# Optimization experiments

Hardware: AMD Instinct MI355X
Metric: run time of the kernel (lower is better)

Reference implementation:

```python
import jax, jax.numpy as jnp
from jax import lax
import numpy as np

TOPN = 6
IOU_THRESH = 0.25
PAD = 224
CROP = 224

def make_edge_anchors():
    # (fm, stride, base_size, scales, ratios): 6 anchors/cell on 14x14 and 7x7, 9 on 4x4
    specs = [(14, 32, 48, [1.0, 1.26], [0.667, 1.0, 1.5]),
             (7, 64, 96, [1.0, 1.26], [0.667, 1.0, 1.5]),
             (4, 112, 192, [1.0, 1.26, 1.59], [0.667, 1.0, 1.5])]
    out = []
    for fm, stride, base, scales, ratios in specs:
        cy = (np.arange(fm) + 0.5) * stride
        yy, xx = np.meshgrid(cy, cy, indexing='ij')
        for s in scales:          # anchor-type-major order matches NCHW flatten of tidy heads
            for r in ratios:
                h = base * s * np.sqrt(r)
                w = base * s / np.sqrt(r)
                b = np.stack([yy - h / 2, xx - w / 2, yy + h / 2, xx + w / 2], -1)
                out.append(b.reshape(-1, 4))
    anchors = np.concatenate(out, 0) + PAD  # shift into padded-image coords
    return np.clip(anchors, 0, 448 + 2 * PAD).astype(np.int32)  # [1614,4]

def conv2d(x, w, b, stride, pad):
    y = lax.conv_general_dilated(x, w, (stride, stride), [(pad, pad), (pad, pad)],
                                 dimension_numbers=('NCHW', 'OIHW', 'NCHW'))
    return y + b[None, :, None, None]

def proposal_net(rpn_feature, w1, b1, w2, b2, w3, b3, tw1, tb1, tw2, tb2, tw3, tb3):
    B = rpn_feature.shape[0]
    d1 = jax.nn.relu(conv2d(rpn_feature, w1, b1, 1, 1))  # [B,128,14,14]
    d2 = jax.nn.relu(conv2d(d1, w2, b2, 2, 1))           # [B,128,7,7]
    d3 = jax.nn.relu(conv2d(d2, w3, b3, 2, 1))           # [B,128,4,4]
    t1 = conv2d(d1, tw1, tb1, 1, 0).reshape(B, -1)       # [B,1176]
    t2 = conv2d(d2, tw2, tb2, 1, 0).reshape(B, -1)       # [B,294]
    t3 = conv2d(d3, tw3, tb3, 1, 0).reshape(B, -1)       # [B,144]
    return jnp.concatenate([t1, t2, t3], axis=1)         # [B,1614]

def hard_nms_indices(scores, boxes_f):
    # scores [N], boxes_f [N,4] float; iterative greedy hard-NMS, returns TOPN indices
    def body(i, carry):
        sc, idxs = carry
        j = jnp.argmax(sc)
        idxs = idxs.at[i].set(j.astype(jnp.int32))
        b = boxes_f[j]
        yy0 = jnp.maximum(b[0], boxes_f[:, 0]); xx0 = jnp.maximum(b[1], boxes_f[:, 1])
        yy1 = jnp.minimum(b[2], boxes_f[:, 2]); xx1 = jnp.minimum(b[3], boxes_f[:, 3])
        inter = jnp.clip(yy1 - yy0, 0) * jnp.clip(xx1 - xx0, 0)
        a1 = (b[2] - b[0]) * (b[3] - b[1])
        a2 = (boxes_f[:, 2] - boxes_f[:, 0]) * (boxes_f[:, 3] - boxes_f[:, 1])
        iou = inter / (a1 + a2 - inter)
        sc = jnp.where(iou > IOU_THRESH, -jnp.inf, sc)  # suppresses chosen box too (iou=1)
        return sc, idxs
    _, idxs = lax.fori_loop(0, TOPN, body, (scores, jnp.zeros(TOPN, jnp.int32)))
    return idxs

def crop_resize_224(img, box):
    # img [3,Hp,Wp], box int [4]=(y0,x0,y1,x1); bilinear, align_corners=True
    Hp, Wp = img.shape[1], img.shape[2]
    y0, x0, y1, x1 = box[0], box[1], box[2], box[3]
    t = jnp.arange(CROP, dtype=jnp.float32) / (CROP - 1)
    ys = y0.astype(jnp.float32) + t * (y1 - y0 - 1).astype(jnp.float32)
    xs = x0.astype(jnp.float32) + t * (x1 - x0 - 1).astype(jnp.float32)
    y0i = jnp.floor(ys).astype(jnp.int32); y1i = jnp.minimum(y0i + 1, Hp - 1)
    x0i = jnp.floor(xs).astype(jnp.int32); x1i = jnp.minimum(x0i + 1, Wp - 1)
    wy = (ys - y0i)[None, :, None]
    wx = (xs - x0i)[None, None, :]
    top = img[:, y0i, :]; bot = img[:, y1i, :]            # [3,224,Wp]
    tl = top[:, :, x0i]; tr = top[:, :, x1i]              # [3,224,224]
    bl = bot[:, :, x0i]; br = bot[:, :, x1i]
    return tl * (1 - wy) * (1 - wx) + tr * (1 - wy) * wx + bl * wy * (1 - wx) + br * wy * wx

def setup_inputs() -> dict:
    key = jax.random.key(0)
    ks = jax.random.split(key, 16)
    B = 16
    s = 0.02
    inp = {
        'x': jax.random.normal(ks[0], (B, 3, 448, 448), jnp.float32),
        'rpn_feature': jax.random.normal(ks[1], (B, 2048, 14, 14), jnp.float32),
        'edge_anchors': jnp.asarray(make_edge_anchors()),
        'w_down1': jax.random.normal(ks[2], (128, 2048, 3, 3), jnp.float32) * s,
        'b_down1': jnp.zeros((128,), jnp.float32),
        'w_down2': jax.random.normal(ks[3], (128, 128, 3, 3), jnp.float32) * s,
        'b_down2': jnp.zeros((128,), jnp.float32),
        'w_down3': jax.random.normal(ks[4], (128, 128, 3, 3), jnp.float32) * s,
        'b_down3': jnp.zeros((128,), jnp.float32),
        'w_tidy1': jax.random.normal(ks[5], (6, 128, 1, 1), jnp.float32) * s,
        'b_tidy1': jnp.zeros((6,), jnp.float32),
        'w_tidy2': jax.random.normal(ks[6], (6, 128, 1, 1), jnp.float32) * s,
        'b_tidy2': jnp.zeros((6,), jnp.float32),
        'w_tidy3': jax.random.normal(ks[7], (9, 128, 1, 1), jnp.float32) * s,
        'b_tidy3': jnp.zeros((9,), jnp.float32),
    }
    return inp

def reference(x, rpn_feature, edge_anchors, w_down1, b_down1, w_down2, b_down2,
              w_down3, b_down3, w_tidy1, b_tidy1, w_tidy2, b_tidy2, w_tidy3, b_tidy3):
    rpn_score = proposal_net(rpn_feature, w_down1, b_down1, w_down2, b_down2,
                             w_down3, b_down3, w_tidy1, b_tidy1, w_tidy2, b_tidy2,
                             w_tidy3, b_tidy3)                      # [B,1614]
    boxes_f = edge_anchors.astype(jnp.float32)
    top_n_index = jax.vmap(lambda sc: hard_nms_indices(sc, boxes_f))(rpn_score)  # [B,TOPN]
    top_n_prob = jnp.take_along_axis(rpn_score, top_n_index, axis=1)             # [B,TOPN]
    x_pad = jnp.pad(x, ((0, 0), (0, 0), (PAD, PAD), (PAD, PAD)))                 # [B,3,896,896]
    sel_boxes = edge_anchors[top_n_index]                                        # [B,TOPN,4]
    part_imgs = jax.vmap(lambda img, bxs: jax.vmap(lambda b: crop_resize_224(img, b))(bxs))(x_pad, sel_boxes)  # [B,TOPN,3,224,224]
    return rpn_score, top_n_index, top_n_prob, part_imgs
```

## Files before the change

kernel.cpp:

```cpp
#include <hip/hip_runtime.h>
#include <hip/hip_bf16.h>
#include <math.h>

#define B 16
#define A 1614
#define S1 1176
#define S2 294
#define S3 144
#define CROP 224
#define PADI 224

typedef __attribute__((ext_vector_type(8))) short short8;
typedef __attribute__((ext_vector_type(4))) float f32x4;

__device__ __forceinline__ unsigned short bf16u(float v) {
    union { __hip_bfloat16 h; unsigned short u; } cv;
    cv.h = __float2bfloat16(v);
    return cv.u;
}
__device__ __forceinline__ float bf16f(unsigned short u) {
    union { unsigned short u; __hip_bfloat16 h; } cv;
    cv.u = u;
    return __bfloat162float(cv.h);
}


__global__ void init_d1_kernel(const float* __restrict__ b1, float* __restrict__ d1) {
    int i = blockIdx.x * 256 + threadIdx.x;
    if (i < B * 128 * 196) d1[i] = b1[(i / 196) & 127];
}

__global__ void pack_w_kernel(const float* __restrict__ w,
                              unsigned short* __restrict__ wh,
                              unsigned short* __restrict__ wl)
{
    int chunk = blockIdx.x * 4 + (threadIdx.x >> 6);
    int lane = threadIdx.x & 63;
    int kidx = chunk & 63;
    int q = chunk >> 6;
    int t = q % 9, ct = q / 9;
    int co = ct * 16 + (lane & 15);
    int ci0 = kidx * 32 + (lane >> 4) * 8;
    short8 h8, l8;
#pragma unroll
    for (int j = 0; j < 8; j++) {
        float v = w[(co * 2048 + ci0 + j) * 9 + t];
        unsigned short h = bf16u(v);
        h8[j] = (short)h;
        l8[j] = (short)bf16u(v - bf16f(h));
    }
    *(short8*)(wh + (size_t)chunk * 512 + lane * 8) = h8;
    *(short8*)(wl + (size_t)chunk * 512 + lane * 8) = l8;
}

__global__ void __launch_bounds__(256, 2)
conv1_mfma_kernel(const float* __restrict__ in,
                  const unsigned short* __restrict__ wh,
                  const unsigned short* __restrict__ wl,
                  float* __restrict__ d1)
{
    __shared__ short lds[32768];
    const int b   = blockIdx.x;
    const int ctg = blockIdx.y;
    const int ks  = blockIdx.z;
    const int tid = threadIdx.x;
    const int wave = tid >> 6, lane = tid & 63;
    const int quad = lane >> 4;

    int bbase[13];
#pragma unroll
    for (int nt = 0; nt < 13; nt++) {
        int pos = nt * 16 + (lane & 15);
        int py = pos / 14, px = pos % 14;
        int plane = (pos < 196) ? ((py + 1) * 16 + (px + 1)) : 17;
        bbase[nt] = plane * 32 + quad * 8;
    }

    f32x4 acc[2][13];
#pragma unroll
    for (int m = 0; m < 2; m++)
#pragma unroll
        for (int nt = 0; nt < 13; nt++)
            acc[m][nt] = (f32x4){0.f, 0.f, 0.f, 0.f};

    for (int i = tid; i < 16384; i += 256) ((int*)lds)[i] = 0;
    __syncthreads();

    const int ci_base = ks * 256;
    for (int g = 0; g < 4; g++) {
        if (g) __syncthreads();
        for (int i = tid; i < 8 * 196; i += 256) {
            int blk = i / 196, p = i - blk * 196;
            int py = p / 14, px = p - py * 14;
            int plane = (py + 1) * 16 + (px + 1);
            const float* src = in + (size_t)(b * 2048 + ci_base + g * 64 + blk * 8) * 196 + p;
            short8 h8, l8;
#pragma unroll
            for (int j = 0; j < 8; j++) {
                float v = src[j * 196];
                unsigned short h = bf16u(v);
                h8[j] = (short)h;
                l8[j] = (short)bf16u(v - bf16f(h));
            }
            int kc = blk >> 2;
            int off = (kc * 256 + plane) * 32 + (blk & 3) * 8;
            *(short8*)&lds[off] = h8;
            *(short8*)&lds[16384 + off] = l8;
        }
        __syncthreads();
        int cls = (wave + g) & 3;
        for (int k = 0; k < 5; k++) {
            int u = k * 4 + cls;
            if (u >= 18) break;
            int tap = u >> 1, kc = u & 1;
            int dy = tap / 3, dx = tap - dy * 3;
            int tapoff = ((dy - 1) * 16 + (dx - 1)) * 32;
            int kidx = ks * 8 + g * 2 + kc;
            size_t c0 = (size_t)(((ctg * 2 + 0) * 9 + tap) * 64 + kidx) * 512 + lane * 8;
            size_t c1 = (size_t)(((ctg * 2 + 1) * 9 + tap) * 64 + kidx) * 512 + lane * 8;
            const short8 ah0 = *(const short8*)(wh + c0);
            const short8 al0 = *(const short8*)(wl + c0);
            const short8 ah1 = *(const short8*)(wh + c1);
            const short8 al1 = *(const short8*)(wl + c1);
#pragma unroll
            for (int nt = 0; nt < 13; nt++) {
                int idx = kc * 8192 + bbase[nt] + tapoff;
                short8 bh = *(const short8*)&lds[idx];
                short8 bl = *(const short8*)&lds[16384 + idx];
                acc[0][nt] = __builtin_amdgcn_mfma_f32_16x16x32_bf16(ah0, bh, acc[0][nt], 0, 0, 0);
                acc[1][nt] = __builtin_amdgcn_mfma_f32_16x16x32_bf16(ah1, bh, acc[1][nt], 0, 0, 0);
                acc[0][nt] = __builtin_amdgcn_mfma_f32_16x16x32_bf16(ah0, bl, acc[0][nt], 0, 0, 0);
                acc[1][nt] = __builtin_amdgcn_mfma_f32_16x16x32_bf16(ah1, bl, acc[1][nt], 0, 0, 0);
                acc[0][nt] = __builtin_amdgcn_mfma_f32_16x16x32_bf16(al0, bh, acc[0][nt], 0, 0, 0);
                acc[1][nt] = __builtin_amdgcn_mfma_f32_16x16x32_bf16(al1, bh, acc[1][nt], 0, 0, 0);
            }
        }
    }

    __syncthreads();
    float* red = (float*)lds;
    for (int w = 0; w < 4; w++) {
        if (wave == w) {
#pragma unroll
            for (int m = 0; m < 2; m++)
#pragma unroll
                for (int nt = 0; nt < 13; nt++)
#pragma unroll
                    for (int r = 0; r < 4; r++) {
                        int slot = ((m * 13 + nt) * 4 + r) * 64 + lane;
                        float v = acc[m][nt][r];
                        if (w == 0) red[slot] = v; else red[slot] += v;
                    }
        }
        __syncthreads();
    }
    for (int s = tid; s < 2 * 13 * 4 * 64; s += 256) {
        int lane_s = s & 63;
        int r = (s >> 6) & 3;
        int nt = (s >> 8) % 13;
        int m = (s >> 8) / 13;
        int pos = nt * 16 + (lane_s & 15);
        if (pos < 196) {
            int co = ctg * 32 + m * 16 + (lane_s >> 4) * 4 + r;
            atomicAdd(&d1[(size_t)(b * 128 + co) * 196 + pos], red[s]);
        }
    }
}

__global__ void trans_d1_kernel(const float* __restrict__ d1, float* __restrict__ d1t)
{
    int i = blockIdx.x * 256 + threadIdx.x;
    int co = i & 127; int t = i >> 7;
    int pos = t % 196; int b = t / 196;
    d1t[i] = fmaxf(d1[(b * 128 + co) * 196 + pos], 0.f);
}

__global__ void __launch_bounds__(256)
conv2_kernel(const float* __restrict__ d1, const float* __restrict__ w,
             const float* __restrict__ bias, float* __restrict__ d2,
             float* __restrict__ d2t)
{
    __shared__ float s1[64 * 196];
    const int b = blockIdx.x, cog = blockIdx.y;
    const int tid = threadIdx.x;
    const int wave = __builtin_amdgcn_readfirstlane(tid >> 6);
    const int lane = tid & 63;
    const int pos = lane;
    const bool act = pos < 49;
    const int oy = pos / 7, ox = pos % 7;

    int off[9]; float msk[9];
#pragma unroll
    for (int dy = 0; dy < 3; dy++)
#pragma unroll
        for (int dx = 0; dx < 3; dx++) {
            int iy = 2 * oy - 1 + dy, ix = 2 * ox - 1 + dx;
            bool v = act && (unsigned)iy < 14u && (unsigned)ix < 14u;
            off[dy * 3 + dx] = v ? iy * 14 + ix : 0;
            msk[dy * 3 + dx] = v ? 1.f : 0.f;
        }

    const int co0 = cog * 16 + wave * 4;
    float acc0 = bias[co0], acc1 = bias[co0 + 1], acc2 = bias[co0 + 2], acc3 = bias[co0 + 3];

    for (int h = 0; h < 2; h++) {
        if (h) __syncthreads();
        for (int i = tid; i < 64 * 196; i += 256)
            s1[i] = fmaxf(d1[b * 25088 + h * 12544 + i], 0.f);
        __syncthreads();
        for (int ci = 0; ci < 64; ci++) {
            const float* base = s1 + ci * 196;
            float t[9];
#pragma unroll
            for (int k = 0; k < 9; k++) t[k] = msk[k] * base[off[k]];
            const int cig = h * 64 + ci;
            const float* wp0 = w + (size_t)((co0    ) * 128 + cig) * 9;
            const float* wp1 = w + (size_t)((co0 + 1) * 128 + cig) * 9;
            const float* wp2 = w + (size_t)((co0 + 2) * 128 + cig) * 9;
            const float* wp3 = w + (size_t)((co0 + 3) * 128 + cig) * 9;
#pragma unroll
            for (int k = 0; k < 9; k++) {
                acc0 = fmaf(t[k], wp0[k], acc0);
                acc1 = fmaf(t[k], wp1[k], acc1);
                acc2 = fmaf(t[k], wp2[k], acc2);
                acc3 = fmaf(t[k], wp3[k], acc3);
            }
        }
    }
    if (act) {
        float r0 = fmaxf(acc0, 0.f), r1 = fmaxf(acc1, 0.f);
        float r2 = fmaxf(acc2, 0.f), r3 = fmaxf(acc3, 0.f);
        d2[(b * 128 + co0    ) * 49 + pos] = r0;
        d2[(b * 128 + co0 + 1) * 49 + pos] = r1;
        d2[(b * 128 + co0 + 2) * 49 + pos] = r2;
        d2[(b * 128 + co0 + 3) * 49 + pos] = r3;
        float* dt = d2t + (b * 49 + pos) * 128 + co0;
        dt[0] = r0; dt[1] = r1; dt[2] = r2; dt[3] = r3;
    }
}

__global__ void __launch_bounds__(256)
conv3_kernel(const float* __restrict__ d2, const float* __restrict__ w,
             const float* __restrict__ bias, float* __restrict__ d3t)
{
    __shared__ float s2[128 * 49];
    const int b = blockIdx.x, cog = blockIdx.y;
    const int tid = threadIdx.x;
    for (int i = tid; i < 128 * 49; i += 256) s2[i] = d2[b * 6272 + i];
    __syncthreads();

    const int co = cog * 16 + (tid >> 4);
    const int pos = tid & 15, oy = pos >> 2, ox = pos & 3;
    int off[9]; float msk[9];
#pragma unroll
    for (int dy = 0; dy < 3; dy++)
#pragma unroll
        for (int dx = 0; dx < 3; dx++) {
            int iy = 2 * oy - 1 + dy, ix = 2 * ox - 1 + dx;
            bool v = (unsigned)iy < 7u && (unsigned)ix < 7u;
            off[dy * 3 + dx] = v ? iy * 7 + ix : 0;
            msk[dy * 3 + dx] = v ? 1.f : 0.f;
        }
    float acc = bias[co];
    const float* wp = w + (size_t)co * 1152;
    for (int ci = 0; ci < 128; ci++) {
        const float* base = s2 + ci * 49;
        const float* wc = wp + ci * 9;
#pragma unroll
        for (int k = 0; k < 9; k++)
            acc = fmaf(msk[k] * base[off[k]], wc[k], acc);
    }
    d3t[(b * 16 + pos) * 128 + co] = fmaxf(acc, 0.f);
}

__global__ void __launch_bounds__(256)
tidy_kernel(const float* __restrict__ d1t, const float* __restrict__ d2t,
            const float* __restrict__ d3t,
            const float* __restrict__ wt1, const float* __restrict__ bt1,
            const float* __restrict__ wt2, const float* __restrict__ bt2,
            const float* __restrict__ wt3, const float* __restrict__ bt3,
            float* __restrict__ scores)
{
    int gw = blockIdx.x * 4 + (threadIdx.x >> 6);
    int lane = threadIdx.x & 63;
    int b = gw / A, s = gw - b * A;
    const float *f, *wv; float bias;
    if (s < S1) {
        int c = s / 196, pos = s - c * 196;
        f = d1t + (b * 196 + pos) * 128; wv = wt1 + c * 128; bias = bt1[c];
    } else if (s < S1 + S2) {
        int u = s - S1; int c = u / 49, pos = u - c * 49;
        f = d2t + (b * 49 + pos) * 128; wv = wt2 + c * 128; bias = bt2[c];
    } else {
        int u = s - S1 - S2; int c = u / 16, pos = u - c * 16;
        f = d3t + (b * 16 + pos) * 128; wv = wt3 + c * 128; bias = bt3[c];
    }
    float a = f[lane] * wv[lane] + f[lane + 64] * wv[lane + 64];
#pragma unroll
    for (int m = 32; m; m >>= 1) a += __shfl_xor(a, m, 64);
    if (lane == 0) scores[gw] = a + bias;
}

__global__ void nms_kernel(const float* __restrict__ scores, const int* __restrict__ anchors,
                           float* __restrict__ out_idx, float* __restrict__ out_prob,
                           int* __restrict__ boxes_out)
{
    __shared__ float sc[A];
    __shared__ float ay0[A], ax0[A], ay1[A], ax1[A], aarea[A];
    __shared__ float rv[256];
    __shared__ int   ri[256];
    __shared__ int   chosen;
    const int b = blockIdx.x, tid = threadIdx.x;

    for (int i = tid; i < A; i += 256) {
        sc[i] = scores[b * A + i];
        int y0 = anchors[i * 4 + 0], x0 = anchors[i * 4 + 1];
        int y1 = anchors[i * 4 + 2], x1 = anchors[i * 4 + 3];
        ay0[i] = (float)y0; ax0[i] = (float)x0;
        ay1[i] = (float)y1; ax1[i] = (float)x1;
        aarea[i] = (float)(y1 - y0) * (float)(x1 - x0);
    }
    __syncthreads();

    for (int it = 0; it < 6; it++) {
        float bv = -INFINITY; int bi = 0x7fffffff;
        for (int i = tid; i < A; i += 256) {
            if (sc[i] > bv) { bv = sc[i]; bi = i; }
        }
        rv[tid] = bv; ri[tid] = bi;
        __syncthreads();
        for (int s = 128; s > 0; s >>= 1) {
            if (tid < s) {
                if (rv[tid + s] > rv[tid] ||
                    (rv[tid + s] == rv[tid] && ri[tid + s] < ri[tid])) {
                    rv[tid] = rv[tid + s]; ri[tid] = ri[tid + s];
                }
            }
            __syncthreads();
        }
        if (tid == 0) {
            int j = ri[0];
            chosen = j;
            out_idx[b * 6 + it]  = (float)j;
            out_prob[b * 6 + it] = rv[0];
            boxes_out[(b * 6 + it) * 4 + 0] = anchors[j * 4 + 0];
            boxes_out[(b * 6 + it) * 4 + 1] = anchors[j * 4 + 1];
            boxes_out[(b * 6 + it) * 4 + 2] = anchors[j * 4 + 2];
            boxes_out[(b * 6 + it) * 4 + 3] = anchors[j * 4 + 3];
        }
        __syncthreads();
        const int j = chosen;
        const float jy0 = ay0[j], jx0 = ax0[j], jy1 = ay1[j], jx1 = ax1[j], ja = aarea[j];
        for (int i = tid; i < A; i += 256) {
            float yy0 = fmaxf(jy0, ay0[i]), xx0 = fmaxf(jx0, ax0[i]);
            float yy1 = fminf(jy1, ay1[i]), xx1 = fminf(jx1, ax1[i]);
            float inter = fmaxf(yy1 - yy0, 0.f) * fmaxf(xx1 - xx0, 0.f);
            float iou = inter / (ja + aarea[i] - inter);
            if (iou > 0.25f) sc[i] = -INFINITY;
        }
        __syncthreads();
    }
}

__device__ __forceinline__ float sample_pad(const float* __restrict__ x,
                                            int bc, int y, int xx)
{
    y -= PADI; xx -= PADI;
    if ((unsigned)y < 448u && (unsigned)xx < 448u)
        return x[(bc * 448 + y) * 448 + xx];
    return 0.f;
}

__global__ void crop_kernel(const float* __restrict__ x, const int* __restrict__ boxes,
                            float* __restrict__ parts)
{
    int idx = blockIdx.x * 256 + threadIdx.x;
    int ix = idx % 224; int t = idx / 224;
    int iy = t % 224;  t /= 224;
    int c  = t % 3;    t /= 3;
    int n  = t % 6;    int b = t / 6;

    const int* bx = boxes + (b * 6 + n) * 4;
    const int y0 = bx[0], x0 = bx[1], y1 = bx[2], x1 = bx[3];

    float ty = (float)iy / 223.f;
    float tx = (float)ix / 223.f;
    float ys = (float)y0 + ty * (float)(y1 - y0 - 1);
    float xs = (float)x0 + tx * (float)(x1 - x0 - 1);
    int y0i = (int)floorf(ys);
    int x0i = (int)floorf(xs);
    float wy = ys - (float)y0i;
    float wx = xs - (float)x0i;
    int y1i = min(y0i + 1, 895);
    int x1i = min(x0i + 1, 895);

    const int bc = b * 3 + c;
    float v00 = sample_pad(x, bc, y0i, x0i);
    float v01 = sample_pad(x, bc, y0i, x1i);
    float v10 = sample_pad(x, bc, y1i, x0i);
    float v11 = sample_pad(x, bc, y1i, x1i);

    float v = v00 * (1.f - wy) * (1.f - wx) + v01 * (1.f - wy) * wx
            + v10 * wy * (1.f - wx)         + v11 * wy * wx;
    parts[idx] = v;
}

extern "C" void kernel_launch(void* const* d_in, const int* in_sizes, int n_in,
                              void* d_out, int out_size, void* d_ws, size_t ws_size,
                              hipStream_t stream)
{
    const float* x       = (const float*)d_in[0];
    const float* rpn     = (const float*)d_in[1];
    const int*   anchors = (const int*)  d_in[2];
    const float* w1  = (const float*)d_in[3];  const float* b1  = (const float*)d_in[4];
    const float* w2  = (const float*)d_in[5];  const float* b2  = (const float*)d_in[6];
    const float* w3  = (const float*)d_in[7];  const float* b3  = (const float*)d_in[8];
    const float* wt1 = (const float*)d_in[9];  const float* bt1 = (const float*)d_in[10];
    const float* wt2 = (const float*)d_in[11]; const float* bt2 = (const float*)d_in[12];
    const float* wt3 = (const float*)d_in[13]; const float* bt3 = (const float*)d_in[14];

    float* out = (float*)d_out;
    float* d1  = (float*)d_ws;
    float* d1t = d1  + 401408;
    float* d2  = d1t + 401408;
    float* d2t = d2  + 100352;
    float* d3t = d2t + 100352;
    int*   boxes = (int*)(d3t + 32768);
    unsigned short* wh = (unsigned short*)((float*)d_ws + 1036672);
    unsigned short* wl = wh + 2359296;

    float* scores = out;
    float* oidx   = out + 25824;
    float* oprob  = out + 25920;
    float* parts  = out + 26016;

    pack_w_kernel<<<1152, 256, 0, stream>>>(w1, wh, wl);
    init_d1_kernel<<<(B * 128 * 196 + 255) / 256, 256, 0, stream>>>(b1, d1);
    conv1_mfma_kernel<<<dim3(16, 4, 8), 256, 0, stream>>>(rpn, wh, wl, d1);
    trans_d1_kernel<<<401408 / 256, 256, 0, stream>>>(d1, d1t);
    conv2_kernel<<<dim3(16, 8), 256, 0, stream>>>(d1, w2, b2, d2, d2t);
    conv3_kernel<<<dim3(16, 8), 256, 0, stream>>>(d2, w3, b3, d3t);
    tidy_kernel<<<25824 / 4, 256, 0, stream>>>(d1t, d2t, d3t,
                                               wt1, bt1, wt2, bt2, wt3, bt3, scores);
    nms_kernel<<<16, 256, 0, stream>>>(scores, anchors, oidx, oprob, boxes);
    crop_kernel<<<(16 * 6 * 3 * 224 * 224) / 256, 256, 0, stream>>>(x, boxes, parts);
}
```

Baseline: 341.3 us.

## Pre-convert conv1 input to padded bf16 planes and stage via direct global-to-LDS loads

Adds a kernel that splits the conv1 input into hi/lo bf16 halves already laid out in the padded LDS plane format. Conv1 then fills LDS with global_load_lds DMA instead of strided fp32 loads and per-block conversion, so each block no longer repeats the conversion work. The weight pack kernel is rewritten to stage weights through LDS for coalesced reads. The cost is an extra launch and a round trip through workspace for the converted input. A fallback path keeps the old kernel when the workspace is too small.

```diff
diff --git a/kernel.cpp b/kernel.cpp
--- a/kernel.cpp
+++ b/kernel.cpp
@@ -24,37 +24,94 @@
     return __bfloat162float(cv.h);
 }
 
+typedef __attribute__((address_space(3))) void lds_t;
+typedef __attribute__((address_space(1))) void glob_t;
+__device__ __forceinline__ void gload_lds16(const void* g, void* l) {
+    __builtin_amdgcn_global_load_lds((const glob_t*)g, (lds_t*)l, 16, 0, 0);
+}
+
 
 __global__ void init_d1_kernel(const float* __restrict__ b1, float* __restrict__ d1) {
     int i = blockIdx.x * 256 + threadIdx.x;
     if (i < B * 128 * 196) d1[i] = b1[(i / 196) & 127];
 }
 
-__global__ void pack_w_kernel(const float* __restrict__ w,
-                              unsigned short* __restrict__ wh,
-                              unsigned short* __restrict__ wl)
-{
-    int chunk = blockIdx.x * 4 + (threadIdx.x >> 6);
-    int lane = threadIdx.x & 63;
-    int kidx = chunk & 63;
-    int q = chunk >> 6;
-    int t = q % 9, ct = q / 9;
-    int co = ct * 16 + (lane & 15);
-    int ci0 = kidx * 32 + (lane >> 4) * 8;
-    short8 h8, l8;
-#pragma unroll
-    for (int j = 0; j < 8; j++) {
-        float v = w[(co * 2048 + ci0 + j) * 9 + t];
-        unsigned short h = bf16u(v);
-        h8[j] = (short)h;
-        l8[j] = (short)bf16u(v - bf16f(h));
-    }
-    *(short8*)(wh + (size_t)chunk * 512 + lane * 8) = h8;
-    *(short8*)(wl + (size_t)chunk * 512 + lane * 8) = l8;
+__global__ void __launch_bounds__(256)
+pack_w_kernel(const float* __restrict__ w,
+              unsigned short* __restrict__ wh,
+              unsigned short* __restrict__ wl)
+{
+    __shared__ float lw[16 * 289];
+    const int blk = blockIdx.x;
+    const int ct = blk >> 6, kidx = blk & 63;
+    const int tid = threadIdx.x;
+    const float* src = w + ((size_t)ct * 16 * 2048 + kidx * 32) * 9;
+    for (int i = tid; i < 4608; i += 256) {
+        int co = i / 288, r = i - co * 288;
+        lw[co * 289 + r] = src[(size_t)co * 18432 + r];
+    }
+    __syncthreads();
+    for (int u = tid; u < 576; u += 256) {
+        int t = u >> 6, lane = u & 63;
+        int co = lane & 15, quad = lane >> 4;
+        short8 h8, l8;
+#pragma unroll
+        for (int j = 0; j < 8; j++) {
+            float v = lw[co * 289 + (quad * 8 + j) * 9 + t];
+            unsigned short h = bf16u(v);
+            h8[j] = (short)h;
+            l8[j] = (short)bf16u(v - bf16f(h));
+        }
+        size_t off = ((size_t)((ct * 9 + t) * 64 + kidx)) * 512 + lane * 8;
+        *(short8*)(wh + off) = h8;
+        *(short8*)(wl + off) = l8;
+    }
+}
+
+__global__ void __launch_bounds__(256)
+cvt_x_kernel(const float* __restrict__ in,
+             unsigned short* __restrict__ xh,
+             unsigned short* __restrict__ xl)
+{
+    __shared__ unsigned short sh[8192], sl[8192];
+    const int blk = blockIdx.x;
+    const int b = blk >> 6, kidx = blk & 63;
+    const int tid = threadIdx.x;
+    for (int i = tid; i < 4096; i += 256) { ((unsigned*)sh)[i] = 0u; ((unsigned*)sl)[i] = 0u; }
+    __syncthreads();
+    const float* src = in + ((size_t)b * 2048 + kidx * 32) * 196;
+    for (int i = tid; i < 1568; i += 256) {
+        int p = i >> 3, cq = i & 7;
+        int plane = (p / 14 + 1) * 16 + (p % 14 + 1);
+        unsigned hv0, hv1, lv0, lv1;
+        unsigned short h[4], l[4];
+#pragma unroll
+        for (int k = 0; k < 4; k++) {
+            float v = src[(size_t)(cq * 4 + k) * 196 + p];
+            unsigned short hh = bf16u(v);
+            h[k] = hh; l[k] = bf16u(v - bf16f(hh));
+        }
+        hv0 = (unsigned)h[0] | ((unsigned)h[1] << 16);
+        hv1 = (unsigned)h[2] | ((unsigned)h[3] << 16);
+        lv0 = (unsigned)l[0] | ((unsigned)l[1] << 16);
+        lv1 = (unsigned)l[2] | ((unsigned)l[3] << 16);
+        unsigned* ph = (unsigned*)&sh[plane * 32 + cq * 4];
+        unsigned* pl = (unsigned*)&sl[plane * 32 + cq * 4];
+        ph[0] = hv0; ph[1] = hv1;
+        pl[0] = lv0; pl[1] = lv1;
+    }
+    __syncthreads();
+    int4* oh = (int4*)(xh + (size_t)blk * 8192);
+    int4* ol = (int4*)(xl + (size_t)blk * 8192);
+    for (int i = tid; i < 1024; i += 256) {
+        oh[i] = ((int4*)sh)[i];
+        ol[i] = ((int4*)sl)[i];
+    }
 }
 
 __global__ void __launch_bounds__(256, 2)
-conv1_mfma_kernel(const float* __restrict__ in,
+conv1_mfma_kernel(const unsigned short* __restrict__ xh,
+                  const unsigned short* __restrict__ xl,
                   const unsigned short* __restrict__ wh,
                   const unsigned short* __restrict__ wl,
                   float* __restrict__ d1)
@@ -83,29 +140,17 @@
         for (int nt = 0; nt < 13; nt++)
             acc[m][nt] = (f32x4){0.f, 0.f, 0.f, 0.f};
 
-    for (int i = tid; i < 16384; i += 256) ((int*)lds)[i] = 0;
-    __syncthreads();
-
-    const int ci_base = ks * 256;
     for (int g = 0; g < 4; g++) {
         if (g) __syncthreads();
-        for (int i = tid; i < 8 * 196; i += 256) {
-            int blk = i / 196, p = i - blk * 196;
-            int py = p / 14, px = p - py * 14;
-            int plane = (py + 1) * 16 + (px + 1);
-            const float* src = in + (size_t)(b * 2048 + ci_base + g * 64 + blk * 8) * 196 + p;
-            short8 h8, l8;
-#pragma unroll
-            for (int j = 0; j < 8; j++) {
-                float v = src[j * 196];
-                unsigned short h = bf16u(v);
-                h8[j] = (short)h;
-                l8[j] = (short)bf16u(v - bf16f(h));
-            }
-            int kc = blk >> 2;
-            int off = (kc * 256 + plane) * 32 + (blk & 3) * 8;
-            *(short8*)&lds[off] = h8;
-            *(short8*)&lds[16384 + off] = l8;
+        const size_t gb = (size_t)(b * 64 + ks * 8 + g * 2) * 16384;
+        const char* sH = (const char*)xh + gb + wave * 8192 + lane * 16;
+        const char* sL = (const char*)xl + gb + wave * 8192 + lane * 16;
+        char* dH = (char*)lds + wave * 8192;
+        char* dL = (char*)lds + 32768 + wave * 8192;
+#pragma unroll
+        for (int t = 0; t < 8; t++) {
+            gload_lds16(sH + t * 1024, dH + t * 1024);
+            gload_lds16(sL + t * 1024, dL + t * 1024);
         }
         __syncthreads();
         int cls = (wave + g) & 3;
@@ -167,6 +212,116 @@
     }
 }
 
+__global__ void __launch_bounds__(256, 2)
+conv1_mfma_fb_kernel(const float* __restrict__ in,
+                     const unsigned short* __restrict__ wh,
+                     const unsigned short* __restrict__ wl,
+                     float* __restrict__ d1)
+{
+    __shared__ short lds[32768];
+    const int b   = blockIdx.x;
+    const int ctg = blockIdx.y;
+    const int ks  = blockIdx.z;
+    const int tid = threadIdx.x;
+    const int wave = tid >> 6, lane = tid & 63;
+    const int quad = lane >> 4;
+
+    int bbase[13];
+#pragma unroll
+    for (int nt = 0; nt < 13; nt++) {
+        int pos = nt * 16 + (lane & 15);
+        int py = pos / 14, px = pos % 14;
+        int plane = (pos < 196) ? ((py + 1) * 16 + (px + 1)) : 17;
+        bbase[nt] = plane * 32 + quad * 8;
+    }
+    f32x4 acc[2][13];
+#pragma unroll
+    for (int m = 0; m < 2; m++)
+#pragma unroll
+        for (int nt = 0; nt < 13; nt++)
+            acc[m][nt] = (f32x4){0.f, 0.f, 0.f, 0.f};
+    for (int i = tid; i < 16384; i += 256) ((int*)lds)[i] = 0;
+    __syncthreads();
+    const int ci_base = ks * 256;
+    for (int g = 0; g < 4; g++) {
+        if (g) __syncthreads();
+        for (int i = tid; i < 8 * 196; i += 256) {
+            int blk = i / 196, p = i - blk * 196;
+            int py = p / 14, px = p - py * 14;
+            int plane = (py + 1) * 16 + (px + 1);
+            const float* src = in + (size_t)(b * 2048 + ci_base + g * 64 + blk * 8) * 196 + p;
+            short8 h8, l8;
+#pragma unroll
+            for (int j = 0; j < 8; j++) {
+                float v = src[j * 196];
+                unsigned short h = bf16u(v);
+                h8[j] = (short)h;
+                l8[j] = (short)bf16u(v - bf16f(h));
+            }
+            int kc = blk >> 2;
+            int off = (kc * 256 + plane) * 32 + (blk & 3) * 8;
+            *(short8*)&lds[off] = h8;
+            *(short8*)&lds[16384 + off] = l8;
+        }
+        __syncthreads();
+        int cls = (wave + g) & 3;
+        for (int k = 0; k < 5; k++) {
+            int u = k * 4 + cls;
+            if (u >= 18) break;
+            int tap = u >> 1, kc = u & 1;
+            int dy = tap / 3, dx = tap - dy * 3;
+            int tapoff = ((dy - 1) * 16 + (dx - 1)) * 32;
+            int kidx = ks * 8 + g * 2 + kc;
+            size_t c0 = (size_t)(((ctg * 2 + 0) * 9 + tap) * 64 + kidx) * 512 + lane * 8;
+            size_t c1 = (size_t)(((ctg * 2 + 1) * 9 + tap) * 64 + kidx) * 512 + lane * 8;
+            const short8 ah0 = *(const short8*)(wh + c0);
+            const short8 al0 = *(const short8*)(wl + c0);
+            const short8 ah1 = *(const short8*)(wh + c1);
+            const short8 al1 = *(const short8*)(wl + c1);
+#pragma unroll
+            for (int nt = 0; nt < 13; nt++) {
+                int idx = kc * 8192 + bbase[nt] + tapoff;
+                short8 bh = *(const short8*)&lds[idx];
+                short8 bl = *(const short8*)&lds[16384 + idx];
+                acc[0][nt] = __builtin_amdgcn_mfma_f32_16x16x32_bf16(ah0, bh, acc[0][nt], 0, 0, 0);
+                acc[1][nt] = __builtin_amdgcn_mfma_f32_16x16x32_bf16(ah1, bh, acc[1][nt], 0, 0, 0);
+                acc[0][nt] = __builtin_amdgcn_mfma_f32_16x16x32_bf16(ah0, bl, acc[0][nt], 0, 0, 0);
+                acc[1][nt] = __builtin_amdgcn_mfma_f32_16x16x32_bf16(ah1, bl, acc[1][nt], 0, 0, 0);
+                acc[0][nt] = __builtin_amdgcn_mfma_f32_16x16x32_bf16(al0, bh, acc[0][nt], 0, 0, 0);
+                acc[1][nt] = __builtin_amdgcn_mfma_f32_16x16x32_bf16(al1, bh, acc[1][nt], 0, 0, 0);
+            }
+        }
+    }
+    __syncthreads();
+    float* red = (float*)lds;
+    for (int w = 0; w < 4; w++) {
+        if (wave == w) {
+#pragma unroll
+            for (int m = 0; m < 2; m++)
+#pragma unroll
+                for (int nt = 0; nt < 13; nt++)
+#pragma unroll
+                    for (int r = 0; r < 4; r++) {
+                        int slot = ((m * 13 + nt) * 4 + r) * 64 + lane;
+                        float v = acc[m][nt][r];
+                        if (w == 0) red[slot] = v; else red[slot] += v;
+                    }
+        }
+        __syncthreads();
+    }
+    for (int s = tid; s < 2 * 13 * 4 * 64; s += 256) {
+        int lane_s = s & 63;
+        int r = (s >> 6) & 3;
+        int nt = (s >> 8) % 13;
+        int m = (s >> 8) / 13;
+        int pos = nt * 16 + (lane_s & 15);
+        if (pos < 196) {
+            int co = ctg * 32 + m * 16 + (lane_s >> 4) * 4 + r;
+            atomicAdd(&d1[(size_t)(b * 128 + co) * 196 + pos], red[s]);
+        }
+    }
+}
+
 __global__ void trans_d1_kernel(const float* __restrict__ d1, float* __restrict__ d1t)
 {
     int i = blockIdx.x * 256 + threadIdx.x;
@@ -420,23 +575,32 @@
     const float* wt3 = (const float*)d_in[13]; const float* bt3 = (const float*)d_in[14];
 
     float* out = (float*)d_out;
-    float* d1  = (float*)d_ws;
+    float* wsf = (float*)d_ws;
+    float* d1  = wsf;
     float* d1t = d1  + 401408;
     float* d2  = d1t + 401408;
     float* d2t = d2  + 100352;
     float* d3t = d2t + 100352;
     int*   boxes = (int*)(d3t + 32768);
-    unsigned short* wh = (unsigned short*)((float*)d_ws + 1036672);
+    unsigned short* wh = (unsigned short*)(wsf + 1036672);
     unsigned short* wl = wh + 2359296;
+    unsigned short* xh = (unsigned short*)((char*)d_ws + 13583872);
+    unsigned short* xl = (unsigned short*)((char*)d_ws + 30361088);
+    const bool big_ws = ws_size >= 47138304ull;
 
     float* scores = out;
     float* oidx   = out + 25824;
     float* oprob  = out + 25920;
     float* parts  = out + 26016;
 
-    pack_w_kernel<<<1152, 256, 0, stream>>>(w1, wh, wl);
+    pack_w_kernel<<<512, 256, 0, stream>>>(w1, wh, wl);
     init_d1_kernel<<<(B * 128 * 196 + 255) / 256, 256, 0, stream>>>(b1, d1);
-    conv1_mfma_kernel<<<dim3(16, 4, 8), 256, 0, stream>>>(rpn, wh, wl, d1);
+    if (big_ws) {
+        cvt_x_kernel<<<1024, 256, 0, stream>>>(rpn, xh, xl);
+        conv1_mfma_kernel<<<dim3(16, 4, 8), 256, 0, stream>>>(xh, xl, wh, wl, d1);
+    } else {
+        conv1_mfma_fb_kernel<<<dim3(16, 4, 8), 256, 0, stream>>>(rpn, wh, wl, d1);
+    }
     trans_d1_kernel<<<401408 / 256, 256, 0, stream>>>(d1, d1t);
     conv2_kernel<<<dim3(16, 8), 256, 0, stream>>>(d1, w2, b2, d2, d2t);
     conv3_kernel<<<dim3(16, 8), 256, 0, stream>>>(d2, w3, b3, d3t);
```

New measurement: 358.5 us. +5.0%, slower.

## Prepack conv1 activations to bf16 hi/lo and stream them via global_load_lds

Applied to the files above, without the earlier changes.

A single prep kernel now packs the weights (transposed through LDS so global reads coalesce), converts the rpn activations into padded bf16 hi/lo tiles in global memory, and initialises d1 with the bias, replacing two separate kernels. Conv1 then copies those pre-laid-out tiles straight into LDS with global_load_lds, using a smaller LDS footprint and prefetching the next tap's weight fragments. The d1 transpose kernel is folded into conv2, which writes d1t while it loads its input. This removes per-block conversion work and two launches, at the cost of extra workspace traffic for the packed activations.

```diff
diff --git a/kernel.cpp b/kernel.cpp
--- a/kernel.cpp
+++ b/kernel.cpp
@@ -24,45 +24,101 @@
     return __bfloat162float(cv.h);
 }
 
-
-__global__ void init_d1_kernel(const float* __restrict__ b1, float* __restrict__ d1) {
-    int i = blockIdx.x * 256 + threadIdx.x;
-    if (i < B * 128 * 196) d1[i] = b1[(i / 196) & 127];
-}
-
-__global__ void pack_w_kernel(const float* __restrict__ w,
-                              unsigned short* __restrict__ wh,
-                              unsigned short* __restrict__ wl)
-{
-    int chunk = blockIdx.x * 4 + (threadIdx.x >> 6);
-    int lane = threadIdx.x & 63;
-    int kidx = chunk & 63;
-    int q = chunk >> 6;
-    int t = q % 9, ct = q / 9;
-    int co = ct * 16 + (lane & 15);
-    int ci0 = kidx * 32 + (lane >> 4) * 8;
-    short8 h8, l8;
-#pragma unroll
-    for (int j = 0; j < 8; j++) {
-        float v = w[(co * 2048 + ci0 + j) * 9 + t];
-        unsigned short h = bf16u(v);
-        h8[j] = (short)h;
-        l8[j] = (short)bf16u(v - bf16f(h));
-    }
-    *(short8*)(wh + (size_t)chunk * 512 + lane * 8) = h8;
-    *(short8*)(wl + (size_t)chunk * 512 + lane * 8) = l8;
+typedef __attribute__((address_space(3))) void lds_t;
+typedef __attribute__((address_space(1))) void glob_t;
+__device__ __forceinline__ void gload_lds16(const void* g, void* l) {
+    __builtin_amdgcn_global_load_lds((const glob_t*)g, (lds_t*)l, 16, 0, 0);
+}
+
+
+__global__ void __launch_bounds__(256)
+prep_kernel(const float* __restrict__ w1, const float* __restrict__ rpn,
+            const float* __restrict__ b1,
+            unsigned short* __restrict__ wh, unsigned short* __restrict__ wl,
+            unsigned short* __restrict__ xh, unsigned short* __restrict__ xl,
+            float* __restrict__ d1)
+{
+    __shared__ char smem[32768];
+    const int bx = blockIdx.x, tid = threadIdx.x;
+
+    if (bx < 512) {
+        float* lw = (float*)smem;
+        const int ct = bx >> 6, kidx = bx & 63;
+        const float* src = w1 + ((size_t)ct * 16 * 2048 + kidx * 32) * 9;
+        for (int i = tid; i < 4608; i += 256) {
+            int co = i / 288, r = i - co * 288;
+            lw[co * 289 + r] = src[(size_t)co * 18432 + r];
+        }
+        __syncthreads();
+        for (int u = tid; u < 576; u += 256) {
+            int t = u >> 6, lane = u & 63;
+            int co = lane & 15, quad = lane >> 4;
+            short8 h8, l8;
+#pragma unroll
+            for (int j = 0; j < 8; j++) {
+                float v = lw[co * 289 + (quad * 8 + j) * 9 + t];
+                unsigned short h = bf16u(v);
+                h8[j] = (short)h;
+                l8[j] = (short)bf16u(v - bf16f(h));
+            }
+            size_t off = ((size_t)((ct * 9 + t) * 64 + kidx)) * 512 + lane * 8;
+            *(short8*)(wh + off) = h8;
+            *(short8*)(wl + off) = l8;
+        }
+    } else if (bx < 1536) {
+        unsigned short* sh = (unsigned short*)smem;
+        unsigned short* sl = (unsigned short*)smem + 8192;
+        const int blk = bx - 512;
+        const int b = blk >> 6, kidx = blk & 63;
+        for (int i = tid; i < 8192; i += 256) ((unsigned*)smem)[i] = 0u;
+        __syncthreads();
+        const float* src = rpn + ((size_t)b * 2048 + kidx * 32) * 196;
+        for (int i = tid; i < 1568; i += 256) {
+            int p = i >> 3, cq = i & 7;
+            int plane = (p / 14 + 1) * 16 + (p % 14 + 1);
+            unsigned short h[4], l[4];
+#pragma unroll
+            for (int k = 0; k < 4; k++) {
+                float v = src[(size_t)(cq * 4 + k) * 196 + p];
+                unsigned short hh = bf16u(v);
+                h[k] = hh; l[k] = bf16u(v - bf16f(hh));
+            }
+            int soff = (cq >> 1) * 2048 + plane * 8 + (cq & 1) * 4;
+            unsigned* ph = (unsigned*)&sh[soff];
+            unsigned* pl = (unsigned*)&sl[soff];
+            ph[0] = (unsigned)h[0] | ((unsigned)h[1] << 16);
+            ph[1] = (unsigned)h[2] | ((unsigned)h[3] << 16);
+            pl[0] = (unsigned)l[0] | ((unsigned)l[1] << 16);
+            pl[1] = (unsigned)l[2] | ((unsigned)l[3] << 16);
+        }
+        __syncthreads();
+        int4* oh = (int4*)(xh + (size_t)blk * 8192);
+        int4* ol = (int4*)(xl + (size_t)blk * 8192);
+        const int4* ih = (const int4*)sh;
+        const int4* il = (const int4*)sl;
+        for (int i = tid; i < 1024; i += 256) { oh[i] = ih[i]; ol[i] = il[i]; }
+    } else {
+        int base = (bx - 1536) * 4096 + tid * 16;
+#pragma unroll
+        for (int j = 0; j < 16; j++) {
+            int idx = base + j;
+            d1[idx] = b1[(idx / 196) & 127];
+        }
+    }
 }
 
 __global__ void __launch_bounds__(256, 2)
-conv1_mfma_kernel(const float* __restrict__ in,
+conv1_mfma_kernel(const unsigned short* __restrict__ xh,
+                  const unsigned short* __restrict__ xl,
                   const unsigned short* __restrict__ wh,
                   const unsigned short* __restrict__ wl,
                   float* __restrict__ d1)
 {
-    __shared__ short lds[32768];
-    const int b   = blockIdx.x;
-    const int ctg = blockIdx.y;
-    const int ks  = blockIdx.z;
+    __shared__ short lds[16384];
+    const int bid = blockIdx.x;
+    const int ctg = bid >> 7;
+    const int pr  = bid & 127;
+    const int b   = pr >> 3, ks = pr & 7;
     const int tid = threadIdx.x;
     const int wave = tid >> 6, lane = tid & 63;
     const int quad = lane >> 4;
@@ -73,7 +129,7 @@
         int pos = nt * 16 + (lane & 15);
         int py = pos / 14, px = pos % 14;
         int plane = (pos < 196) ? ((py + 1) * 16 + (px + 1)) : 17;
-        bbase[nt] = plane * 32 + quad * 8;
+        bbase[nt] = quad * 2048 + plane * 8;
     }
 
     f32x4 acc[2][13];
@@ -83,50 +139,47 @@
         for (int nt = 0; nt < 13; nt++)
             acc[m][nt] = (f32x4){0.f, 0.f, 0.f, 0.f};
 
-    for (int i = tid; i < 16384; i += 256) ((int*)lds)[i] = 0;
-    __syncthreads();
-
-    const int ci_base = ks * 256;
-    for (int g = 0; g < 4; g++) {
+    for (int g = 0; g < 8; g++) {
         if (g) __syncthreads();
-        for (int i = tid; i < 8 * 196; i += 256) {
-            int blk = i / 196, p = i - blk * 196;
-            int py = p / 14, px = p - py * 14;
-            int plane = (py + 1) * 16 + (px + 1);
-            const float* src = in + (size_t)(b * 2048 + ci_base + g * 64 + blk * 8) * 196 + p;
-            short8 h8, l8;
-#pragma unroll
-            for (int j = 0; j < 8; j++) {
-                float v = src[j * 196];
-                unsigned short h = bf16u(v);
-                h8[j] = (short)h;
-                l8[j] = (short)bf16u(v - bf16f(h));
-            }
-            int kc = blk >> 2;
-            int off = (kc * 256 + plane) * 32 + (blk & 3) * 8;
-            *(short8*)&lds[off] = h8;
-            *(short8*)&lds[16384 + off] = l8;
-        }
-        __syncthreads();
-        int cls = (wave + g) & 3;
-        for (int k = 0; k < 5; k++) {
-            int u = k * 4 + cls;
-            if (u >= 18) break;
-            int tap = u >> 1, kc = u & 1;
-            int dy = tap / 3, dx = tap - dy * 3;
-            int tapoff = ((dy - 1) * 16 + (dx - 1)) * 32;
-            int kidx = ks * 8 + g * 2 + kc;
-            size_t c0 = (size_t)(((ctg * 2 + 0) * 9 + tap) * 64 + kidx) * 512 + lane * 8;
-            size_t c1 = (size_t)(((ctg * 2 + 1) * 9 + tap) * 64 + kidx) * 512 + lane * 8;
-            const short8 ah0 = *(const short8*)(wh + c0);
-            const short8 al0 = *(const short8*)(wl + c0);
-            const short8 ah1 = *(const short8*)(wh + c1);
-            const short8 al1 = *(const short8*)(wl + c1);
+        const size_t cb = (size_t)(b * 64 + ks * 8 + g) * 8192;
+        const char* sH = (const char*)(xh + cb) + wave * 4096 + lane * 16;
+        const char* sL = (const char*)(xl + cb) + wave * 4096 + lane * 16;
+        char* dH = (char*)lds + wave * 4096;
+        char* dL = (char*)lds + 16384 + wave * 4096;
+#pragma unroll
+        for (int t = 0; t < 4; t++) {
+            gload_lds16(sH + t * 1024, dH + t * 1024);
+            gload_lds16(sL + t * 1024, dL + t * 1024);
+        }
+        __syncthreads();
+
+        const int kidx = ks * 8 + g;
+        const int cls = (wave + g) & 3;
+        int u = cls;
+        size_t cA0 = (size_t)(((ctg * 2 + 0) * 9 + u) * 64 + kidx) * 512 + lane * 8;
+        size_t cA1 = (size_t)(((ctg * 2 + 1) * 9 + u) * 64 + kidx) * 512 + lane * 8;
+        short8 ah0 = *(const short8*)(wh + cA0);
+        short8 al0 = *(const short8*)(wl + cA0);
+        short8 ah1 = *(const short8*)(wh + cA1);
+        short8 al1 = *(const short8*)(wl + cA1);
+        while (u < 9) {
+            const int un = u + 4;
+            short8 nh0, nl0, nh1, nl1;
+            if (un < 9) {
+                size_t nB0 = (size_t)(((ctg * 2 + 0) * 9 + un) * 64 + kidx) * 512 + lane * 8;
+                size_t nB1 = (size_t)(((ctg * 2 + 1) * 9 + un) * 64 + kidx) * 512 + lane * 8;
+                nh0 = *(const short8*)(wh + nB0);
+                nl0 = *(const short8*)(wl + nB0);
+                nh1 = *(const short8*)(wh + nB1);
+                nl1 = *(const short8*)(wl + nB1);
+            }
+            const int dy = u / 3, dx = u - dy * 3;
+            const int poff = ((dy - 1) * 16 + (dx - 1)) * 8;
 #pragma unroll
             for (int nt = 0; nt < 13; nt++) {
-                int idx = kc * 8192 + bbase[nt] + tapoff;
+                int idx = bbase[nt] + poff;
                 short8 bh = *(const short8*)&lds[idx];
-                short8 bl = *(const short8*)&lds[16384 + idx];
+                short8 bl = *(const short8*)&lds[8192 + idx];
                 acc[0][nt] = __builtin_amdgcn_mfma_f32_16x16x32_bf16(ah0, bh, acc[0][nt], 0, 0, 0);
                 acc[1][nt] = __builtin_amdgcn_mfma_f32_16x16x32_bf16(ah1, bh, acc[1][nt], 0, 0, 0);
                 acc[0][nt] = __builtin_amdgcn_mfma_f32_16x16x32_bf16(ah0, bl, acc[0][nt], 0, 0, 0);
@@ -134,6 +187,8 @@
                 acc[0][nt] = __builtin_amdgcn_mfma_f32_16x16x32_bf16(al0, bh, acc[0][nt], 0, 0, 0);
                 acc[1][nt] = __builtin_amdgcn_mfma_f32_16x16x32_bf16(al1, bh, acc[1][nt], 0, 0, 0);
             }
+            u = un;
+            if (u < 9) { ah0 = nh0; al0 = nl0; ah1 = nh1; al1 = nl1; }
         }
     }
 
@@ -167,18 +222,10 @@
     }
 }
 
-__global__ void trans_d1_kernel(const float* __restrict__ d1, float* __restrict__ d1t)
-{
-    int i = blockIdx.x * 256 + threadIdx.x;
-    int co = i & 127; int t = i >> 7;
-    int pos = t % 196; int b = t / 196;
-    d1t[i] = fmaxf(d1[(b * 128 + co) * 196 + pos], 0.f);
-}
-
 __global__ void __launch_bounds__(256)
 conv2_kernel(const float* __restrict__ d1, const float* __restrict__ w,
              const float* __restrict__ bias, float* __restrict__ d2,
-             float* __restrict__ d2t)
+             float* __restrict__ d2t, float* __restrict__ d1t)
 {
     __shared__ float s1[64 * 196];
     const int b = blockIdx.x, cog = blockIdx.y;
@@ -205,8 +252,14 @@
 
     for (int h = 0; h < 2; h++) {
         if (h) __syncthreads();
-        for (int i = tid; i < 64 * 196; i += 256)
-            s1[i] = fmaxf(d1[b * 25088 + h * 12544 + i], 0.f);
+        for (int i = tid; i < 64 * 196; i += 256) {
+            float v = fmaxf(d1[b * 25088 + h * 12544 + i], 0.f);
+            s1[i] = v;
+            if (cog == 0) {
+                int ci = i / 196, pp = i - ci * 196;
+                d1t[(b * 196 + pp) * 128 + h * 64 + ci] = v;
+            }
+        }
         __syncthreads();
         for (int ci = 0; ci < 64; ci++) {
             const float* base = s1 + ci * 196;
@@ -420,25 +473,26 @@
     const float* wt3 = (const float*)d_in[13]; const float* bt3 = (const float*)d_in[14];
 
     float* out = (float*)d_out;
-    float* d1  = (float*)d_ws;
+    float* wsf = (float*)d_ws;
+    float* d1  = wsf;
     float* d1t = d1  + 401408;
     float* d2  = d1t + 401408;
     float* d2t = d2  + 100352;
     float* d3t = d2t + 100352;
     int*   boxes = (int*)(d3t + 32768);
-    unsigned short* wh = (unsigned short*)((float*)d_ws + 1036672);
+    unsigned short* wh = (unsigned short*)(wsf + 1036672);
     unsigned short* wl = wh + 2359296;
+    unsigned short* xh = (unsigned short*)((char*)d_ws + 13583872);
+    unsigned short* xl = (unsigned short*)((char*)d_ws + 30361088);
 
     float* scores = out;
     float* oidx   = out + 25824;
     float* oprob  = out + 25920;
     float* parts  = out + 26016;
 
-    pack_w_kernel<<<1152, 256, 0, stream>>>(w1, wh, wl);
-    init_d1_kernel<<<(B * 128 * 196 + 255) / 256, 256, 0, stream>>>(b1, d1);
-    conv1_mfma_kernel<<<dim3(16, 4, 8), 256, 0, stream>>>(rpn, wh, wl, d1);
-    trans_d1_kernel<<<401408 / 256, 256, 0, stream>>>(d1, d1t);
-    conv2_kernel<<<dim3(16, 8), 256, 0, stream>>>(d1, w2, b2, d2, d2t);
+    prep_kernel<<<1634, 256, 0, stream>>>(w1, rpn, b1, wh, wl, xh, xl, d1);
+    conv1_mfma_kernel<<<512, 256, 0, stream>>>(xh, xl, wh, wl, d1);
+    conv2_kernel<<<dim3(16, 8), 256, 0, stream>>>(d1, w2, b2, d2, d2t, d1t);
     conv3_kernel<<<dim3(16, 8), 256, 0, stream>>>(d2, w3, b3, d3t);
     tidy_kernel<<<25824 / 4, 256, 0, stream>>>(d1t, d2t, d3t,
                                                wt1, bt1, wt2, bt2, wt3, bt3, scores);
```

Result: slower. 372.0 us (+9.0%).
